# Performance work log

Hardware: AMD Instinct MI355X
Metric: run time of the kernel (lower is better)

## Reference

```python
import jax, jax.numpy as jnp
import numpy as np

FEAT_STRIDE = 16
SCORE_THRESH = 0.7
DIST_THRESH = 16.0
MAX_OUT = 50
B = 2048
IMG_W = 65536


def setup_inputs() -> dict:
    key = jax.random.key(0)
    k1, k2, k3 = jax.random.split(key, 3)
    fw = IMG_W // FEAT_STRIDE
    pred_cls_logit = jax.random.normal(k1, (B, fw), dtype=jnp.float32)
    pred_delta = jax.random.normal(k2, (B, fw, 2), dtype=jnp.float32)
    # realistic image widths in [0.5, 1.0] * img_width
    real_images_width = jax.random.uniform(k3, (B,), jnp.float32, 0.5, 1.0) * IMG_W
    return {
        "pred_cls_logit": pred_cls_logit,
        "pred_delta": pred_delta,
        "img_width": IMG_W,
        "real_images_width": real_images_width,
    }


def _nms_one(positions, scores):
    # positions: [N, 2], scores: [N]. Greedy 1D NMS, fixed MAX_OUT iterations.
    centers = positions.mean(axis=1)                      # [N]
    alive0 = scores >= SCORE_THRESH                       # score-threshold filter

    def step(alive, _):
        masked = jnp.where(alive, scores, -1e30)
        i = jnp.argmax(masked)                            # highest remaining score
        has = jnp.any(alive)
        f = has.astype(jnp.float32)                       # 1.0 if a box was picked
        p = positions[i] * f
        s = scores[i] * f
        # suppress everything within DIST_THRESH of picked center (incl. itself)
        new_alive = alive & (jnp.abs(centers - centers[i]) > DIST_THRESH)
        return new_alive, (p, s, f)

    _, (P, S, F) = jax.lax.scan(step, alive0, None, length=MAX_OUT)
    # pad_to_fixed_size: append validity flag column, zero-padded rows
    nms_positions = jnp.concatenate([P, F[:, None]], axis=1)   # [MAX_OUT, 3]
    nms_scores = jnp.concatenate([S[:, None], F[:, None]], axis=1)  # [MAX_OUT, 2]
    return nms_positions, nms_scores


def reference(pred_cls_logit, pred_delta, img_width, real_images_width):
    feat_width = img_width // FEAT_STRIDE
    interval_center = (jnp.arange(feat_width, dtype=jnp.float32) + 0.5) * FEAT_STRIDE
    # [B, feat_width, 2]
    pos = pred_delta * FEAT_STRIDE + interval_center[None, :, None]
    scores = jax.nn.sigmoid(pred_cls_logit)               # [B, feat_width]
    max_width = real_images_width[:, None, None] - 1.0
    pos = jnp.where(pos < 0.0, 0.0, pos)
    pos = jnp.where(pos > max_width, max_width, pos)

    nms_positions, nms_scores = jax.vmap(_nms_one)(pos, scores)

    nms_center = nms_positions[..., :2].mean(axis=2)      # [B, MAX_OUT]
    x_interval_num = jnp.floor(nms_center / FEAT_STRIDE).astype(jnp.int32)
    valid = nms_positions[..., 2] == 1.0
    idx = jnp.where(valid, x_interval_num, feat_width)    # out-of-range -> dropped
    cls_ids = jax.vmap(
        lambda ii: jnp.zeros((feat_width,), jnp.float32).at[ii].set(1.0, mode='drop')
    )(idx)                                                # [B, feat_width]
    return nms_positions, nms_scores, cls_ids
```

## Files before the change

kernel.cpp:

```cpp
#include <hip/hip_runtime.h>
#include <math.h>

#define FW 4096
#define SEG 256
#define SEGCAP 96
#define NSEG 16
#define NSLOT (NSEG * SEGCAP)
#define MAX_OUT 50
#define NJ 24


template <int CTRL>
__device__ __forceinline__ float dpp_maxf(float v) {
  const int o = __builtin_amdgcn_update_dpp(__float_as_int(v), __float_as_int(v),
                                            CTRL, 0xF, 0xF, false);
  return fmaxf(v, __int_as_float(o));
}
template <int CTRL>
__device__ __forceinline__ unsigned dpp_minu(unsigned v) {
  const unsigned o = (unsigned)__builtin_amdgcn_update_dpp((int)v, (int)v,
                                                           CTRL, 0xF, 0xF, false);
  return (o < v) ? o : v;
}
__device__ __forceinline__ float wave_maxf(float v) {
  v = dpp_maxf<0xB1>(v);
  v = dpp_maxf<0x4E>(v);
  v = dpp_maxf<0x141>(v);
  v = dpp_maxf<0x140>(v);
  v = fmaxf(v, __int_as_float(
          __builtin_amdgcn_ds_swizzle(__float_as_int(v), 0x401F)));
  v = fmaxf(v, __shfl_xor(v, 32, 64));
  return v;
}
__device__ __forceinline__ unsigned wave_minu(unsigned v) {
  v = dpp_minu<0xB1>(v);
  v = dpp_minu<0x4E>(v);
  v = dpp_minu<0x141>(v);
  v = dpp_minu<0x140>(v);
  unsigned o = (unsigned)__builtin_amdgcn_ds_swizzle((int)v, 0x401F);
  v = (o < v) ? o : v;
  o = (unsigned)__shfl_xor((int)v, 32, 64);
  v = (o < v) ? o : v;
  return v;
}

__global__ __launch_bounds__(256) void essp_k1(
    const float* __restrict__ logits,
    const float* __restrict__ deltas,
    const float* __restrict__ realw,
    float* stage)
{
  __shared__ float Lx[4][SEGCAP];
  __shared__ int   Li[4][SEGCAP];

  const int blk  = blockIdx.x;
  const int row  = blk >> 2;
  const int w    = threadIdx.x >> 6;
  const int lane = threadIdx.x & 63;
  const int segr = ((blk & 3) << 2) | w;

  const float mw = realw[row] - 1.0f;
  const float* lgr = logits + (size_t)row * FW + segr * SEG;
  const float4 lx = *(const float4*)(lgr + 4 * lane);
  const float xs[4] = {lx.x, lx.y, lx.z, lx.w};

  bool c[4];
  unsigned long long m[4];
  #pragma unroll
  for (int e = 0; e < 4; ++e) { c[e] = (xs[e] >= 0.846f); m[e] = __ballot(c[e]); }
  const unsigned long long below = (1ULL << lane) - 1ULL;
  int base = __popcll(m[0] & below) + __popcll(m[1] & below)
           + __popcll(m[2] & below) + __popcll(m[3] & below);
  int off = 0;
  #pragma unroll
  for (int e = 0; e < 4; ++e) {
    if (c[e]) {
      const int slot = base + off;
      if (slot < SEGCAP) { Lx[w][slot] = xs[e]; Li[w][slot] = segr * SEG + 4 * lane + e; }
      ++off;
    }
  }
  const int cnt = __popcll(m[0]) + __popcll(m[1]) + __popcll(m[2]) + __popcll(m[3]);
  const int nc = (cnt < SEGCAP) ? cnt : SEGCAP;

  float* Srow = stage + (size_t)row * FW;
  unsigned short* idxrow = (unsigned short*)(Srow + 3072);
  const float* dlr = deltas + (size_t)row * (2 * FW);

  #pragma unroll
  for (int r2 = 0; r2 < 2; ++r2) {
    const int k = lane + 64 * r2;
    if (k < SEGCAP) {
      const int slot = segr * SEGCAP + k;
      float score = -1e30f, cen = 0.0f;
      int idx = 0;
      if (k < nc) {
        const float x = Lx[w][k];
        idx = Li[w][k];
        const float2 d = *(const float2*)(dlr + 2 * idx);
        const float ic = ((float)idx + 0.5f) * 16.0f;
        float p0 = d.x * 16.0f + ic;
        float p1 = d.y * 16.0f + ic;
        p0 = (p0 < 0.f) ? 0.f : p0;  p0 = (p0 > mw) ? mw : p0;
        p1 = (p1 < 0.f) ? 0.f : p1;  p1 = (p1 > mw) ? mw : p1;
        cen = (p0 + p1) * 0.5f;
        const float s = (float)(1.0 / (1.0 + exp(-(double)x)));
        score = (s >= 0.7f) ? s : -1e30f;
      }
      Srow[slot]         = score;
      Srow[1536 + slot]  = cen;
      idxrow[slot]       = (unsigned short)idx;
    }
  }
}

__global__ __launch_bounds__(64) void essp_k2(
    const float* __restrict__ deltas,
    const float* __restrict__ realw,
    float* out_pos,
    float* out_scr,
    float* cls_all)
{
  __shared__ float Lcen[NSLOT];
  __shared__ int   Lpk[MAX_OUT];
  __shared__ float Lps[MAX_OUT];

  const int row  = blockIdx.x;
  const int lane = threadIdx.x;
  float* Srow = cls_all + (size_t)row * FW;

  float sv[NJ], cv[NJ];
  #pragma unroll
  for (int j = 0; j < NJ; ++j) {
    sv[j] = Srow[64 * j + lane];
    cv[j] = Srow[1536 + 64 * j + lane];
    Lcen[64 * j + lane] = cv[j];
  }
  if (lane < MAX_OUT) Lpk[lane] = -1;

  #pragma unroll 1
  for (int it = 0; it < MAX_OUT; ++it) {
    float best = fmaxf(sv[0], sv[1]);
    #pragma unroll
    for (int j = 2; j < NJ; ++j) best = fmaxf(best, sv[j]);
    best = wave_maxf(best);

    unsigned t[NJ];
    #pragma unroll
    for (int j = 0; j < NJ; ++j)
      t[j] = (sv[j] == best) ? (unsigned)(64 * j + lane) : 0x7fffffffu;
    #pragma unroll
    for (int st = 1; st < NJ; st <<= 1) {
      #pragma unroll
      for (int j = 0; j + st < NJ; j += 2 * st)
        t[j] = (t[j + st] < t[j]) ? t[j + st] : t[j];
    }
    const unsigned slotv = wave_minu(t[0]);

    const bool valid = (best >= 0.7f);
    const int slotc = (slotv < NSLOT) ? (int)slotv : (NSLOT - 1);
    float wc = Lcen[slotc];
    wc = valid ? wc : 3.0e38f;
    if (lane == 0) { Lpk[it] = valid ? (int)slotv : -1; Lps[it] = best; }

    #pragma unroll
    for (int j = 0; j < NJ; ++j)
      if (fabsf(cv[j] - wc) <= 16.0f) sv[j] = -1e30f;
  }

  int slot = -1;
  float p0 = 0.f, p1 = 0.f, sc = 0.f;
  int ci = -1;
  if (lane < MAX_OUT) { slot = Lpk[lane]; sc = Lps[lane]; }
  if (slot >= 0) {
    const int idx = ((const unsigned short*)(Srow + 3072))[slot];
    const float2 d = *(const float2*)(deltas + (size_t)row * (2 * FW) + 2 * idx);
    const float mw = realw[row] - 1.0f;
    const float ic = ((float)idx + 0.5f) * 16.0f;
    p0 = d.x * 16.0f + ic;
    p1 = d.y * 16.0f + ic;
    p0 = (p0 < 0.f) ? 0.f : p0;  p0 = (p0 > mw) ? mw : p0;
    p1 = (p1 < 0.f) ? 0.f : p1;  p1 = (p1 > mw) ? mw : p1;
    ci = (int)floorf(Lcen[slot] * 0.0625f);
  }
  asm volatile("s_waitcnt vmcnt(0)" ::: "memory");

  const float4 z4 = make_float4(0.f, 0.f, 0.f, 0.f);
  #pragma unroll
  for (int q = 0; q < 16; ++q)
    *(float4*)(Srow + 256 * q + 4 * lane) = z4;
  asm volatile("s_waitcnt vmcnt(0)" ::: "memory");

  float* prow = out_pos + (size_t)row * (MAX_OUT * 3);
  float* srow = out_scr + (size_t)row * (MAX_OUT * 2);
  if (lane < MAX_OUT) {
    if (slot >= 0) {
      prow[3 * lane + 0] = p0;
      prow[3 * lane + 1] = p1;
      prow[3 * lane + 2] = 1.0f;
      srow[2 * lane + 0] = sc;
      srow[2 * lane + 1] = 1.0f;
      if (ci >= 0 && ci < FW) Srow[ci] = 1.0f;
    } else {
      prow[3 * lane + 0] = 0.0f;
      prow[3 * lane + 1] = 0.0f;
      prow[3 * lane + 2] = 0.0f;
      srow[2 * lane + 0] = 0.0f;
      srow[2 * lane + 1] = 0.0f;
    }
  }
}

extern "C" void kernel_launch(void* const* d_in, const int* in_sizes, int n_in,
                              void* d_out, int out_size, void* d_ws, size_t ws_size,
                              hipStream_t stream) {
  const float* logits = (const float*)d_in[0];
  const float* deltas = (const float*)d_in[1];
  const float* realw  = (const float*)d_in[3];
  const int Bn = in_sizes[3];
  float* out_pos = (float*)d_out;
  float* out_scr = out_pos + (size_t)Bn * MAX_OUT * 3;
  float* out_cls = out_scr + (size_t)Bn * MAX_OUT * 2;

  essp_k1<<<Bn * 4, 256, 0, stream>>>(logits, deltas, realw, out_cls);
  essp_k2<<<Bn, 64, 0, stream>>>(deltas, realw, out_pos, out_scr, out_cls);
}
```

Measured before the change: 79.81 us.

## Fuse argmax score and index into one DPP reduction, keep picks in registers

```diff
diff --git a/kernel.cpp b/kernel.cpp
--- a/kernel.cpp
+++ b/kernel.cpp
@@ -9,40 +9,6 @@
 #define MAX_OUT 50
 #define NJ 24
 
-
-template <int CTRL>
-__device__ __forceinline__ float dpp_maxf(float v) {
-  const int o = __builtin_amdgcn_update_dpp(__float_as_int(v), __float_as_int(v),
-                                            CTRL, 0xF, 0xF, false);
-  return fmaxf(v, __int_as_float(o));
-}
-template <int CTRL>
-__device__ __forceinline__ unsigned dpp_minu(unsigned v) {
-  const unsigned o = (unsigned)__builtin_amdgcn_update_dpp((int)v, (int)v,
-                                                           CTRL, 0xF, 0xF, false);
-  return (o < v) ? o : v;
-}
-__device__ __forceinline__ float wave_maxf(float v) {
-  v = dpp_maxf<0xB1>(v);
-  v = dpp_maxf<0x4E>(v);
-  v = dpp_maxf<0x141>(v);
-  v = dpp_maxf<0x140>(v);
-  v = fmaxf(v, __int_as_float(
-          __builtin_amdgcn_ds_swizzle(__float_as_int(v), 0x401F)));
-  v = fmaxf(v, __shfl_xor(v, 32, 64));
-  return v;
-}
-__device__ __forceinline__ unsigned wave_minu(unsigned v) {
-  v = dpp_minu<0xB1>(v);
-  v = dpp_minu<0x4E>(v);
-  v = dpp_minu<0x141>(v);
-  v = dpp_minu<0x140>(v);
-  unsigned o = (unsigned)__builtin_amdgcn_ds_swizzle((int)v, 0x401F);
-  v = (o < v) ? o : v;
-  o = (unsigned)__shfl_xor((int)v, 32, 64);
-  v = (o < v) ? o : v;
-  return v;
-}
 
 __global__ __launch_bounds__(256) void essp_k1(
     const float* __restrict__ logits,
@@ -114,66 +80,98 @@
   }
 }
 
-__global__ __launch_bounds__(64) void essp_k2(
+template <int CTRL>
+__device__ __forceinline__ void dpp_comb2(float& s, unsigned& k) {
+  const float os = __int_as_float(__builtin_amdgcn_update_dpp(
+      __float_as_int(s), __float_as_int(s), CTRL, 0xF, 0xF, false));
+  const unsigned ok = (unsigned)__builtin_amdgcn_update_dpp(
+      (int)k, (int)k, CTRL, 0xF, 0xF, false);
+  const bool t = (os > s) || (os == s && ok < k);
+  s = t ? os : s;  k = t ? ok : k;
+}
+struct SK { float s; unsigned k; };
+__device__ __forceinline__ SK sk_merge(SK a, SK b) {
+  const bool t = (b.s > a.s) || (b.s == a.s && b.k < a.k);
+  SK r; r.s = t ? b.s : a.s; r.k = t ? b.k : a.k; return r;
+}
+__device__ __forceinline__ SK sk_read(float s, unsigned k, int l) {
+  SK r;
+  r.s = __int_as_float(__builtin_amdgcn_readlane(__float_as_int(s), l));
+  r.k = (unsigned)__builtin_amdgcn_readlane((int)k, l);
+  return r;
+}
+
+__global__ __launch_bounds__(64, 2) void essp_k2(
     const float* __restrict__ deltas,
     const float* __restrict__ realw,
     float* out_pos,
     float* out_scr,
     float* cls_all)
 {
-  __shared__ float Lcen[NSLOT];
-  __shared__ int   Lpk[MAX_OUT];
-  __shared__ float Lps[MAX_OUT];
+  __shared__ float Lce[NSLOT];
 
   const int row  = blockIdx.x;
   const int lane = threadIdx.x;
+  const int l4   = 4 * lane;
   float* Srow = cls_all + (size_t)row * FW;
 
   float sv[NJ], cv[NJ];
   #pragma unroll
-  for (int j = 0; j < NJ; ++j) {
-    sv[j] = Srow[64 * j + lane];
-    cv[j] = Srow[1536 + 64 * j + lane];
-    Lcen[64 * j + lane] = cv[j];
-  }
-  if (lane < MAX_OUT) Lpk[lane] = -1;
+  for (int q = 0; q < 6; ++q) {
+    const float4 s4 = *(const float4*)(Srow + 256 * q + l4);
+    const float4 e4 = *(const float4*)(Srow + 1536 + 256 * q + l4);
+    sv[4*q+0] = s4.x; sv[4*q+1] = s4.y; sv[4*q+2] = s4.z; sv[4*q+3] = s4.w;
+    cv[4*q+0] = e4.x; cv[4*q+1] = e4.y; cv[4*q+2] = e4.z; cv[4*q+3] = e4.w;
+    *(float4*)(&Lce[256 * q + l4]) = e4;
+  }
+
+  int pkv = -1;
+  float psv = 0.f;
 
   #pragma unroll 1
   for (int it = 0; it < MAX_OUT; ++it) {
-    float best = fmaxf(sv[0], sv[1]);
-    #pragma unroll
-    for (int j = 2; j < NJ; ++j) best = fmaxf(best, sv[j]);
-    best = wave_maxf(best);
-
+    float tm[NJ];
+    #pragma unroll
+    for (int j = 0; j < NJ; ++j) tm[j] = sv[j];
+    #pragma unroll
+    for (int st = 1; st < NJ; st <<= 1) {
+      #pragma unroll
+      for (int j = 0; j + st < NJ; j += 2 * st) tm[j] = fmaxf(tm[j], tm[j + st]);
+    }
+    const float best = tm[0];
     unsigned t[NJ];
     #pragma unroll
     for (int j = 0; j < NJ; ++j)
-      t[j] = (sv[j] == best) ? (unsigned)(64 * j + lane) : 0x7fffffffu;
+      t[j] = (sv[j] == best) ? (unsigned)(256 * (j >> 2) + l4 + (j & 3))
+                             : 0x7fffffffu;
     #pragma unroll
     for (int st = 1; st < NJ; st <<= 1) {
       #pragma unroll
       for (int j = 0; j + st < NJ; j += 2 * st)
         t[j] = (t[j + st] < t[j]) ? t[j + st] : t[j];
     }
-    const unsigned slotv = wave_minu(t[0]);
-
-    const bool valid = (best >= 0.7f);
-    const int slotc = (slotv < NSLOT) ? (int)slotv : (NSLOT - 1);
-    float wc = Lcen[slotc];
+    float s = best; unsigned k = t[0];
+    dpp_comb2<0xB1>(s, k);
+    dpp_comb2<0x4E>(s, k);
+    dpp_comb2<0x141>(s, k);
+    dpp_comb2<0x140>(s, k);
+    const SK R = sk_merge(sk_merge(sk_read(s, k, 0),  sk_read(s, k, 16)),
+                          sk_merge(sk_read(s, k, 32), sk_read(s, k, 48)));
+
+    const bool valid = (R.s >= 0.7f);
+    const int kc = (R.k < NSLOT) ? (int)R.k : (NSLOT - 1);
+    float wc = Lce[kc];
     wc = valid ? wc : 3.0e38f;
-    if (lane == 0) { Lpk[it] = valid ? (int)slotv : -1; Lps[it] = best; }
-
+    if (lane == it) { pkv = valid ? (int)R.k : -1; psv = R.s; }
     #pragma unroll
     for (int j = 0; j < NJ; ++j)
       if (fabsf(cv[j] - wc) <= 16.0f) sv[j] = -1e30f;
   }
 
-  int slot = -1;
-  float p0 = 0.f, p1 = 0.f, sc = 0.f;
+  float p0 = 0.f, p1 = 0.f;
   int ci = -1;
-  if (lane < MAX_OUT) { slot = Lpk[lane]; sc = Lps[lane]; }
-  if (slot >= 0) {
-    const int idx = ((const unsigned short*)(Srow + 3072))[slot];
+  if (pkv >= 0) {
+    const int idx = ((const unsigned short*)(Srow + 3072))[pkv];
     const float2 d = *(const float2*)(deltas + (size_t)row * (2 * FW) + 2 * idx);
     const float mw = realw[row] - 1.0f;
     const float ic = ((float)idx + 0.5f) * 16.0f;
@@ -181,24 +179,24 @@
     p1 = d.y * 16.0f + ic;
     p0 = (p0 < 0.f) ? 0.f : p0;  p0 = (p0 > mw) ? mw : p0;
     p1 = (p1 < 0.f) ? 0.f : p1;  p1 = (p1 > mw) ? mw : p1;
-    ci = (int)floorf(Lcen[slot] * 0.0625f);
+    ci = (int)floorf(((p0 + p1) * 0.5f) * 0.0625f);
   }
   asm volatile("s_waitcnt vmcnt(0)" ::: "memory");
 
   const float4 z4 = make_float4(0.f, 0.f, 0.f, 0.f);
   #pragma unroll
   for (int q = 0; q < 16; ++q)
-    *(float4*)(Srow + 256 * q + 4 * lane) = z4;
+    *(float4*)(Srow + 256 * q + l4) = z4;
   asm volatile("s_waitcnt vmcnt(0)" ::: "memory");
 
   float* prow = out_pos + (size_t)row * (MAX_OUT * 3);
   float* srow = out_scr + (size_t)row * (MAX_OUT * 2);
   if (lane < MAX_OUT) {
-    if (slot >= 0) {
+    if (pkv >= 0) {
       prow[3 * lane + 0] = p0;
       prow[3 * lane + 1] = p1;
       prow[3 * lane + 2] = 1.0f;
-      srow[2 * lane + 0] = sc;
+      srow[2 * lane + 0] = psv;
       srow[2 * lane + 1] = 1.0f;
       if (ci >= 0 && ci < FW) Srow[ci] = 1.0f;
     } else {
```

Result: slower. 98.03 us (+22.8%).
